# Kernel optimization log

Hardware: AMD Instinct MI355X
Metric: run time of the kernel (lower is better)

The kernel has to match this reference:

```python
import jax, jax.numpy as jnp
import numpy as np

# Module hyperparameters
P_, K_, NH = 8, 4, 8
B, H, W, C = 2, 64, 24, 256


def setup_inputs() -> dict:
    key = jax.random.key(0)
    ks = jax.random.split(key, 16)

    def w(k, shape, s=0.02):
        return (jax.random.normal(k, shape) * s).astype(jnp.float32)

    z = lambda *shape: jnp.zeros(shape, jnp.float32)
    return {
        'x_2d': jax.random.normal(ks[0], (B, H, W, C), dtype=jnp.float32),
        # block projections (used as x @ W + b)
        'wq_proj': w(ks[1], (C, C)), 'bq_proj': z(C),
        'wk_proj': w(ks[2], (C, C)), 'bk_proj': z(C),
        'wv_proj': w(ks[3], (C, C)), 'bv_proj': z(C),
        # routing attention projections
        'wq_a': w(ks[4], (C, C)), 'bq_a': z(C),
        'wk_a': w(ks[5], (C, C)), 'bk_a': z(C),
        'wv_a': w(ks[6], (C, C)), 'bv_a': z(C),
        'wo_a': w(ks[7], (C, C)), 'bo_a': z(C),
        # global conv path (HWIO, 5x5, SAME padding == torch padding=2)
        'conv_w': w(ks[8], (5, 5, C, C)), 'conv_b': z(C),
        # layer norms
        'ln1_g': jnp.ones((C,), jnp.float32), 'ln1_b': z(C),
        'ln2_g': jnp.ones((C,), jnp.float32), 'ln2_b': z(C),
    }


def _layer_norm(t, g, b, eps=1e-5):
    m = t.mean(-1, keepdims=True)
    v = ((t - m) ** 2).mean(-1, keepdims=True)
    return (t - m) / jnp.sqrt(v + eps) * g + b


def reference(x_2d, wq_proj, bq_proj, wk_proj, bk_proj, wv_proj, bv_proj,
              wq_a, bq_a, wk_a, bk_a, wv_a, bv_a, wo_a, bo_a,
              conv_w, conv_b, ln1_g, ln1_b, ln2_g, ln2_b):
    Bb, Hh, Ww, Cc = x_2d.shape
    hp = Hh // P_                      # block height
    dk = Cc // NH
    kv = min(K_, P_)

    x_p = x_2d.reshape(Bb, P_, hp, Ww, Cc)
    q_p = x_p @ wq_proj + bq_proj
    k_p = x_p @ wk_proj + bk_proj
    v_p = x_p @ wv_proj + bv_proj

    # block-level routing: mean-pooled block descriptors -> top-k blocks
    q_loc = q_p.mean((2, 3))           # [B,P,C]
    k_loc = k_p.mean((2, 3))
    S_loc = jnp.einsum('bpc,bqc->bpq', q_loc, k_loc)
    _, R = jax.lax.top_k(S_loc, kv)    # [B,P,kv] int32 indices into P

    # gather routed K/V blocks: [B,P,kv,hp*W,C]
    k_flat = k_p.reshape(Bb, P_, hp * Ww, Cc)
    v_flat = v_p.reshape(Bb, P_, hp * Ww, Cc)
    k_fil = jax.vmap(lambda t, r: t[r])(k_flat, R).reshape(Bb, P_, kv, hp, Ww, Cc)
    v_fil = jax.vmap(lambda t, r: t[r])(v_flat, R).reshape(Bb, P_, kv, hp, Ww, Cc)
    q_un = jnp.broadcast_to(q_p[:, :, None], (Bb, P_, kv, hp, Ww, Cc))

    # multi-head attention over flattened (kv*hp*W) per block p
    L = kv * hp * Ww
    def to_heads(t, w, b):
        t = t @ w + b
        t = t.reshape(Bb, P_, kv, hp, Ww, NH, dk)
        return t.transpose(0, 5, 1, 2, 3, 4, 6).reshape(Bb, NH, P_, L, dk)

    qh = to_heads(q_un, wq_a, bq_a)
    kh = to_heads(k_fil, wk_a, bk_a)
    vh = to_heads(v_fil, wv_a, bv_a)

    scores = jnp.einsum('bhpqd,bhpkd->bhpqk', qh, kh) / jnp.sqrt(jnp.float32(dk))
    attn = jax.nn.softmax(scores, axis=-1)
    ctx = jnp.einsum('bhpqk,bhpkd->bhpqd', attn, vh)
    # 'b h p (k hp w) dk -> b p k hp w (h dk)'
    ctx = ctx.reshape(Bb, NH, P_, kv, hp, Ww, dk).transpose(0, 2, 3, 4, 5, 1, 6)
    ctx = ctx.reshape(Bb, P_, kv, hp, Ww, Cc)
    routing_out = (ctx @ wo_a + bo_a).mean(2)          # [B,P,hp,W,C]

    x_res = _layer_norm(x_p + routing_out, ln1_g, ln1_b)

    # global conv path (NHWC SAME conv, kernel 5)
    kv_g = (k_p + v_p).reshape(Bb, Hh, Ww, Cc)
    g = jax.lax.conv_general_dilated(kv_g, conv_w, (1, 1), 'SAME',
                                     dimension_numbers=('NHWC', 'HWIO', 'NHWC')) + conv_b
    g = g.reshape(Bb, P_, hp, Ww, Cc)

    out = _layer_norm(x_res + g, ln2_g, ln2_b)
    return out.reshape(Bb, Hh, Ww, Cc)
```

## Files before the change

### kernel.cpp

```cpp
#include <hip/hip_runtime.h>
#include <hip/hip_bf16.h>


#define NPOS 3072
#define CD   256
#define NE   (NPOS*CD)

typedef short bf16x8 __attribute__((ext_vector_type(8)));
typedef float f32x4  __attribute__((ext_vector_type(4)));

__device__ inline ushort f2bf(float f) {
    __hip_bfloat16 h = __float2bfloat16(f);
    return *reinterpret_cast<ushort*>(&h);
}
__device__ inline float bf2f(ushort u) {
    unsigned v = ((unsigned)u) << 16;
    return *reinterpret_cast<float*>(&v);
}

__global__ __launch_bounds__(256) void wtrans7(
    const float* __restrict__ w0, const float* __restrict__ w1, const float* __restrict__ w2,
    const float* __restrict__ w3, const float* __restrict__ w4, const float* __restrict__ w5,
    const float* __restrict__ w6, ushort* __restrict__ wt)
{
    __shared__ float l[64*65];
    int mat = blockIdx.y;
    const float* Wm = mat==0?w0:mat==1?w1:mat==2?w2:mat==3?w3:mat==4?w4:mat==5?w5:w6;
    int r2 = blockIdx.x;
    int ci0 = (r2 >> 2)*64, co0 = (r2 & 3)*64;
    int tid = threadIdx.x, a = tid >> 6, c = tid & 63;
    #pragma unroll 4
    for (int k = 0; k < 16; ++k) {
        int cil = k*4 + a;
        l[cil*65 + c] = Wm[(size_t)(ci0 + cil)*256 + co0 + c];
    }
    __syncthreads();
    #pragma unroll 4
    for (int k = 0; k < 16; ++k) {
        int col = k*4 + a;
        wt[(size_t)mat*65536 + ((size_t)(co0 + col))*256 + ci0 + c] = f2bf(l[c*65 + col]);
    }
}

__global__ __launch_bounds__(256) void wtrans(
    const float* __restrict__ cw, ushort* __restrict__ wct)
{
    __shared__ float l[64*65];
    int blk = blockIdx.x;
    int tap = blk >> 4;
    int r2  = blk & 15;
    int ci0 = (r2 >> 2) * 64;
    int co0 = (r2 & 3) * 64;
    int tid = threadIdx.x;
    int a = tid >> 6;
    int c = tid & 63;
    #pragma unroll 4
    for (int k = 0; k < 16; ++k) {
        int cil = k*4 + a;
        l[cil*65 + c] = cw[(size_t)tap*65536 + (size_t)(ci0 + cil)*256 + co0 + c];
    }
    __syncthreads();
    #pragma unroll 4
    for (int k = 0; k < 16; ++k) {
        int col = k*4 + a;
        wct[((size_t)(tap*256 + co0 + col))*256 + ci0 + c] = f2bf(l[c*65 + col]);
    }
}

__global__ __launch_bounds__(256) void qkloc2(
    const float* __restrict__ x,
    const float* __restrict__ wq, const float* __restrict__ bq,
    const float* __restrict__ wk, const float* __restrict__ bk,
    float* __restrict__ qloc, float* __restrict__ kloc)
{
    __shared__ float xs[256];
    int bp = blockIdx.x, c = threadIdx.x;
    float s = 0.f;
    for (int i = 0; i < 192; ++i)
        s += x[((size_t)(bp*192 + i))*256 + c];
    xs[c] = s * (1.0f/192.0f);
    __syncthreads();
    const float* W  = blockIdx.y ? wk : wq;
    const float* Bv = blockIdx.y ? bk : bq;
    float* dst      = blockIdx.y ? kloc : qloc;
    float acc = Bv[c];
    #pragma unroll 8
    for (int k = 0; k < 256; ++k)
        acc += xs[k] * W[(size_t)k*256 + c];
    dst[bp*256 + c] = acc;
}

__global__ void topk_kern(const float* __restrict__ qloc, const float* __restrict__ kloc,
                          int* __restrict__ Rix)
{
    __shared__ float S[64];
    int b = blockIdx.x, t = threadIdx.x;
    int p = t >> 3, qq = t & 7;
    float s = 0.f;
    for (int c = 0; c < 256; ++c)
        s += qloc[(b*8+p)*256 + c] * kloc[(b*8+qq)*256 + c];
    S[t] = s;
    __syncthreads();
    if (t < 8) {
        float vals[8];
        #pragma unroll
        for (int j = 0; j < 8; ++j) vals[j] = S[t*8 + j];
        for (int j = 0; j < 4; ++j) {
            int best = 0; float bv = vals[0];
            #pragma unroll
            for (int i = 1; i < 8; ++i) if (vals[i] > bv) { bv = vals[i]; best = i; }
            Rix[(b*8 + t)*4 + j] = best;
            vals[best] = -1e30f;
        }
    }
}

__global__ __launch_bounds__(256) void gemm_btx3(
    const float* __restrict__ A,
    const ushort* __restrict__ T0, const ushort* __restrict__ T1, const ushort* __restrict__ T2,
    const float* __restrict__ B0, const float* __restrict__ B1, const float* __restrict__ B2,
    ushort* __restrict__ U0, ushort* __restrict__ U1, ushort* __restrict__ U2)
{
    __shared__ __align__(16) ushort As[32*264];
    int y = blockIdx.y;
    const ushort* T = y==0 ? T0 : (y==1 ? T1 : T2);
    const float* Bi = y==0 ? B0 : (y==1 ? B1 : B2);
    ushort* U = y==0 ? U0 : (y==1 ? U1 : U2);
    int tid = threadIdx.x;
    int m0 = blockIdx.x*32;
    #pragma unroll
    for (int i = 0; i < 4; ++i) {
        int c = i*256 + tid;
        int pos = c >> 5, off = (c & 31)*8;
        const float* src = A + (size_t)(m0 + pos)*256 + off;
        float4 v0 = *(const float4*)src;
        float4 v1 = *(const float4*)(src + 4);
        ushort4 o0, o1;
        o0.x = f2bf(v0.x); o0.y = f2bf(v0.y); o0.z = f2bf(v0.z); o0.w = f2bf(v0.w);
        o1.x = f2bf(v1.x); o1.y = f2bf(v1.y); o1.z = f2bf(v1.z); o1.w = f2bf(v1.w);
        *(ushort4*)&As[pos*264 + off]     = o0;
        *(ushort4*)&As[pos*264 + off + 4] = o1;
    }
    __syncthreads();
    int w = tid >> 6, lane = tid & 63, lm = lane & 15, lq = lane >> 4;
    const ushort* tb = T + ((size_t)(w*64 + lm))*256 + lq*8;

    f32x4 acc[2][4];
    #pragma unroll
    for (int mt = 0; mt < 2; ++mt)
        #pragma unroll
        for (int nt = 0; nt < 4; ++nt) acc[mt][nt] = (f32x4){0.f,0.f,0.f,0.f};

    bf16x8 bw[4];
    #pragma unroll
    for (int nt = 0; nt < 4; ++nt) bw[nt] = *(const bf16x8*)(tb + nt*4096);

    for (int kc = 0; kc < 8; ++kc) {
        int nk = (kc + 1 < 8) ? kc + 1 : 7;
        bf16x8 bn[4];
        #pragma unroll
        for (int nt = 0; nt < 4; ++nt) bn[nt] = *(const bf16x8*)(tb + nt*4096 + nk*32);
        bf16x8 af[2];
        #pragma unroll
        for (int mt = 0; mt < 2; ++mt)
            af[mt] = *(const bf16x8*)&As[(mt*16 + lm)*264 + kc*32 + lq*8];
        #pragma unroll
        for (int mt = 0; mt < 2; ++mt)
            #pragma unroll
            for (int nt = 0; nt < 4; ++nt)
                acc[mt][nt] = __builtin_amdgcn_mfma_f32_16x16x32_bf16(af[mt], bw[nt], acc[mt][nt], 0,0,0);
        #pragma unroll
        for (int nt = 0; nt < 4; ++nt) bw[nt] = bn[nt];
    }

    #pragma unroll
    for (int mt = 0; mt < 2; ++mt) {
        #pragma unroll
        for (int nt = 0; nt < 4; ++nt) {
            int n = w*64 + nt*16 + lm;
            float bb = Bi[n];
            #pragma unroll
            for (int j = 0; j < 4; ++j) {
                int m = m0 + mt*16 + lq*4 + j;
                U[(size_t)m*256 + n] = f2bf(acc[mt][nt][j] + bb);
            }
        }
    }
}

__global__ __launch_bounds__(256) void gemm_bt3(
    const ushort* __restrict__ A0, const ushort* __restrict__ A1, const ushort* __restrict__ A2,
    const ushort* __restrict__ T0, const ushort* __restrict__ T1, const ushort* __restrict__ T2,
    const float* __restrict__ B0, const float* __restrict__ B1, const float* __restrict__ B2,
    ushort* __restrict__ U0, ushort* __restrict__ U1, ushort* __restrict__ U2,
    float s0, float s1, float s2)
{
    __shared__ __align__(16) ushort As[32*264];
    int y = blockIdx.y;
    const ushort* A = y==0 ? A0 : (y==1 ? A1 : A2);
    const ushort* T = y==0 ? T0 : (y==1 ? T1 : T2);
    const float* Bi = y==0 ? B0 : (y==1 ? B1 : B2);
    ushort* U = y==0 ? U0 : (y==1 ? U1 : U2);
    float  sc = y==0 ? s0 : (y==1 ? s1 : s2);
    int tid = threadIdx.x;
    int m0 = blockIdx.x*32;
    #pragma unroll
    for (int i = 0; i < 4; ++i) {
        int c = i*256 + tid;
        int pos = c >> 5, off = (c & 31)*8;
        *(bf16x8*)&As[pos*264 + off] = *(const bf16x8*)(A + (size_t)(m0 + pos)*256 + off);
    }
    __syncthreads();
    int w = tid >> 6, lane = tid & 63, lm = lane & 15, lq = lane >> 4;
    const ushort* tb = T + ((size_t)(w*64 + lm))*256 + lq*8;

    f32x4 acc[2][4];
    #pragma unroll
    for (int mt = 0; mt < 2; ++mt)
        #pragma unroll
        for (int nt = 0; nt < 4; ++nt) acc[mt][nt] = (f32x4){0.f,0.f,0.f,0.f};

    bf16x8 bw[4];
    #pragma unroll
    for (int nt = 0; nt < 4; ++nt) bw[nt] = *(const bf16x8*)(tb + nt*4096);

    for (int kc = 0; kc < 8; ++kc) {
        int nk = (kc + 1 < 8) ? kc + 1 : 7;
        bf16x8 bn[4];
        #pragma unroll
        for (int nt = 0; nt < 4; ++nt) bn[nt] = *(const bf16x8*)(tb + nt*4096 + nk*32);
        bf16x8 af[2];
        #pragma unroll
        for (int mt = 0; mt < 2; ++mt)
            af[mt] = *(const bf16x8*)&As[(mt*16 + lm)*264 + kc*32 + lq*8];
        #pragma unroll
        for (int mt = 0; mt < 2; ++mt)
            #pragma unroll
            for (int nt = 0; nt < 4; ++nt)
                acc[mt][nt] = __builtin_amdgcn_mfma_f32_16x16x32_bf16(af[mt], bw[nt], acc[mt][nt], 0,0,0);
        #pragma unroll
        for (int nt = 0; nt < 4; ++nt) bw[nt] = bn[nt];
    }

    #pragma unroll
    for (int mt = 0; mt < 2; ++mt) {
        #pragma unroll
        for (int nt = 0; nt < 4; ++nt) {
            int n = w*64 + nt*16 + lm;
            float bb = Bi[n];
            #pragma unroll
            for (int j = 0; j < 4; ++j) {
                int m = m0 + mt*16 + lq*4 + j;
                U[(size_t)m*256 + n] = f2bf((acc[mt][nt][j] + bb) * sc);
            }
        }
    }
}

__global__ __launch_bounds__(256) void attn_mfma2(
    const ushort* __restrict__ qab, const ushort* __restrict__ kab,
    const ushort* __restrict__ vab, const int* __restrict__ Rix,
    float* __restrict__ pl, float* __restrict__ pacc)
{
    __shared__ ushort P[4][16*40];
    __shared__ ushort Vs[32*200];
    int tid = threadIdx.x, w = tid >> 6, lane = tid & 63;
    int lm = lane & 15, lq = lane >> 4;
    int bph = blockIdx.x, kvb = blockIdx.y;
    int bp = bph >> 3, h = bph & 7, b = bp >> 3;
    int r = Rix[bp*4 + kvb];
    int vrow0 = (b*8 + r)*192;

    #pragma unroll
    for (int i = 0; i < 6; ++i) {
        int idx = i*256 + tid;
        int pos = idx >> 3, c4 = (idx & 7)*4;
        ushort4 v = *(const ushort4*)(vab + ((size_t)(vrow0 + pos))*256 + h*32 + c4);
        Vs[(c4+0)*200 + pos] = v.x;
        Vs[(c4+1)*200 + pos] = v.y;
        Vs[(c4+2)*200 + pos] = v.z;
        Vs[(c4+3)*200 + pos] = v.w;
    }

    bf16x8 qf[3];
    #pragma unroll
    for (int t = 0; t < 3; ++t)
        qf[t] = *(const bf16x8*)(qab + ((size_t)(bp*192 + w*48 + t*16 + lm))*256 + h*32 + lq*8);

    const ushort* kbase = kab + ((size_t)(vrow0))*256 + h*32 + lq*8;
    ushort* pw = P[w];
    __syncthreads();

    f32x4 O[3][2];
    #pragma unroll
    for (int t = 0; t < 3; ++t) { O[t][0] = (f32x4){0,0,0,0}; O[t][1] = (f32x4){0,0,0,0}; }
    float l[3] = {0.f, 0.f, 0.f};

    for (int k0 = 0; k0 < 192; k0 += 32) {
        bf16x8 kf0 = *(const bf16x8*)(kbase + (size_t)(k0 + lm)*256);
        bf16x8 kf1 = *(const bf16x8*)(kbase + (size_t)(k0 + 16 + lm)*256);
        bf16x8 vf0 = *(const bf16x8*)(&Vs[lm*200 + k0 + lq*8]);
        bf16x8 vf1 = *(const bf16x8*)(&Vs[(16 + lm)*200 + k0 + lq*8]);
        #pragma unroll
        for (int t = 0; t < 3; ++t) {
            f32x4 s0 = __builtin_amdgcn_mfma_f32_16x16x32_bf16(kf0, qf[t], (f32x4){0,0,0,0}, 0,0,0);
            f32x4 s1 = __builtin_amdgcn_mfma_f32_16x16x32_bf16(kf1, qf[t], (f32x4){0,0,0,0}, 0,0,0);
            float p0[4], p1[4];
            #pragma unroll
            for (int j = 0; j < 4; ++j) { p0[j] = __expf(s0[j]); p1[j] = __expf(s1[j]); }
            l[t] += p0[0]+p0[1]+p0[2]+p0[3] + p1[0]+p1[1]+p1[2]+p1[3];
            ushort4 a, c;
            a.x = f2bf(p0[0]); a.y = f2bf(p0[1]); a.z = f2bf(p0[2]); a.w = f2bf(p0[3]);
            c.x = f2bf(p1[0]); c.y = f2bf(p1[1]); c.z = f2bf(p1[2]); c.w = f2bf(p1[3]);
            *(ushort4*)(pw + lm*40 + lq*4)      = a;
            *(ushort4*)(pw + lm*40 + 16 + lq*4) = c;
            bf16x8 pf = *(const bf16x8*)(pw + lm*40 + lq*8);
            O[t][0] = __builtin_amdgcn_mfma_f32_16x16x32_bf16(pf, vf0, O[t][0], 0,0,0);
            O[t][1] = __builtin_amdgcn_mfma_f32_16x16x32_bf16(pf, vf1, O[t][1], 0,0,0);
        }
    }

    #pragma unroll
    for (int t = 0; t < 3; ++t) {
        float lt = l[t];
        lt += __shfl_xor(lt, 16);
        lt += __shfl_xor(lt, 32);
        size_t pbase = ((size_t)(bph*4 + kvb))*192 + w*48 + t*16;
        if (lq == 0) pl[pbase + lm] = lt;
        #pragma unroll
        for (int nt = 0; nt < 2; ++nt)
            #pragma unroll
            for (int reg = 0; reg < 4; ++reg)
                pacc[(pbase + lq*4 + reg)*32 + nt*16 + lm] = O[t][nt][reg];
    }
}

__global__ __launch_bounds__(256) void gemm_wo_ln(
    const float* __restrict__ pl, const float* __restrict__ pacc,
    const ushort* __restrict__ T, const float* __restrict__ boa,
    const float* __restrict__ x,
    const float* __restrict__ g1, const float* __restrict__ b1,
    float* __restrict__ x_res)
{
    __shared__ __align__(16) ushort As[32*264];
    __shared__ float L2x[32*256];
    int tid = threadIdx.x;
    int m0 = blockIdx.x*32;
    #pragma unroll
    for (int i = 0; i < 4; ++i) {
        int c = i*256 + tid;
        int pos = c >> 5, off = (c & 31)*8;
        int m = m0 + pos;
        int bp = m / 192, q = m - bp*192;
        int h = off >> 5, d0 = off & 31;
        int bph = bp*8 + h;
        float ls = 0.f;
        float cv[8] = {0,0,0,0,0,0,0,0};
        #pragma unroll
        for (int k = 0; k < 4; ++k) {
            size_t pidx = ((size_t)(bph*4 + k))*192 + q;
            ls += pl[pidx];
            float4 a0 = *(const float4*)(pacc + pidx*32 + d0);
            float4 a1 = *(const float4*)(pacc + pidx*32 + d0 + 4);
            cv[0] += a0.x; cv[1] += a0.y; cv[2] += a0.z; cv[3] += a0.w;
            cv[4] += a1.x; cv[5] += a1.y; cv[6] += a1.z; cv[7] += a1.w;
        }
        ushort o[8];
        #pragma unroll
        for (int j = 0; j < 8; ++j) o[j] = f2bf(cv[j] / ls);
        *(ushort4*)&As[pos*264 + off]     = make_ushort4(o[0],o[1],o[2],o[3]);
        *(ushort4*)&As[pos*264 + off + 4] = make_ushort4(o[4],o[5],o[6],o[7]);
    }
    __syncthreads();
    int w = tid >> 6, lane = tid & 63, lm = lane & 15, lq = lane >> 4;
    const ushort* tb = T + ((size_t)(w*64 + lm))*256 + lq*8;

    f32x4 acc[2][4];
    #pragma unroll
    for (int mt = 0; mt < 2; ++mt)
        #pragma unroll
        for (int nt = 0; nt < 4; ++nt) acc[mt][nt] = (f32x4){0.f,0.f,0.f,0.f};

    bf16x8 bw[4];
    #pragma unroll
    for (int nt = 0; nt < 4; ++nt) bw[nt] = *(const bf16x8*)(tb + nt*4096);

    for (int kc = 0; kc < 8; ++kc) {
        int nk = (kc + 1 < 8) ? kc + 1 : 7;
        bf16x8 bn[4];
        #pragma unroll
        for (int nt = 0; nt < 4; ++nt) bn[nt] = *(const bf16x8*)(tb + nt*4096 + nk*32);
        bf16x8 af[2];
        #pragma unroll
        for (int mt = 0; mt < 2; ++mt)
            af[mt] = *(const bf16x8*)&As[(mt*16 + lm)*264 + kc*32 + lq*8];
        #pragma unroll
        for (int mt = 0; mt < 2; ++mt)
            #pragma unroll
            for (int nt = 0; nt < 4; ++nt)
                acc[mt][nt] = __builtin_amdgcn_mfma_f32_16x16x32_bf16(af[mt], bw[nt], acc[mt][nt], 0,0,0);
        #pragma unroll
        for (int nt = 0; nt < 4; ++nt) bw[nt] = bn[nt];
    }

    #pragma unroll
    for (int mt = 0; mt < 2; ++mt) {
        #pragma unroll
        for (int nt = 0; nt < 4; ++nt) {
            int n = w*64 + nt*16 + lm;
            float bb = boa[n];
            #pragma unroll
            for (int j = 0; j < 4; ++j) {
                int pos = mt*16 + lq*4 + j;
                float val = acc[mt][nt][j] + bb;
                L2x[pos*256 + n] = val + x[(size_t)(m0 + pos)*256 + n];
            }
        }
    }
    __syncthreads();
    #pragma unroll
    for (int rr = 0; rr < 8; ++rr) {
        int pos = w*8 + rr;
        float4 a = *(const float4*)(&L2x[pos*256 + lane*4]);
        float x0 = a.x, x1 = a.y, x2 = a.z, x3 = a.w;
        float s  = x0 + x1 + x2 + x3;
        float sq = x0*x0 + x1*x1 + x2*x2 + x3*x3;
        #pragma unroll
        for (int off = 32; off > 0; off >>= 1) {
            s  += __shfl_xor(s,  off);
            sq += __shfl_xor(sq, off);
        }
        float mean = s * (1.0f/256.0f);
        float var  = sq * (1.0f/256.0f) - mean*mean;
        float rstd = rsqrtf(var + 1e-5f);
        float4 gv = *(const float4*)(g1 + lane*4);
        float4 bv = *(const float4*)(b1 + lane*4);
        float4 o;
        o.x = (x0 - mean)*rstd*gv.x + bv.x;
        o.y = (x1 - mean)*rstd*gv.y + bv.y;
        o.z = (x2 - mean)*rstd*gv.z + bv.z;
        o.w = (x3 - mean)*rstd*gv.w + bv.w;
        *(float4*)(x_res + (size_t)(m0 + pos)*256 + lane*4) = o;
    }
}

__global__ __launch_bounds__(256) void addkv_pad2(
    const ushort* __restrict__ kpb, const ushort* __restrict__ vpb, ushort* __restrict__ kvb)
{
    int t  = blockIdx.x*256 + threadIdx.x;
    int ci = (t & 63) * 4;
    int p  = t >> 6;
    int xp = p % 28;
    int rr = p / 28;
    int yp = rr % 68;
    int b  = rr / 68;
    int y = yp - 2, x = xp - 2;
    ushort4 o; o.x = 0; o.y = 0; o.z = 0; o.w = 0;
    if (y >= 0 && y < 64 && x >= 0 && x < 24) {
        size_t base = ((size_t)((b*64 + y)*24 + x))*256 + ci;
        ushort4 a = *(const ushort4*)(kpb + base);
        ushort4 c = *(const ushort4*)(vpb + base);
        o.x = f2bf(bf2f(a.x) + bf2f(c.x));
        o.y = f2bf(bf2f(a.y) + bf2f(c.y));
        o.z = f2bf(bf2f(a.z) + bf2f(c.z));
        o.w = f2bf(bf2f(a.w) + bf2f(c.w));
    }
    *(ushort4*)(kvb + (size_t)p*256 + ci) = o;
}

__global__ __launch_bounds__(256) void conv_mfma5(
    const ushort* __restrict__ kvb, const ushort* __restrict__ wct,
    float* __restrict__ pconv)
{
    __shared__ __align__(16) ushort Arows[2][9504];
    int tid = threadIdx.x;
    int bid = blockIdx.x;
    int ch = bid & 1;
    int t2 = bid >> 1;
    int rp = t2 / 5, dy = t2 - rp*5;
    int b = rp >> 5, y0 = (rp & 31)*2;

    const ushort* src0 = kvb + ((size_t)((b*68 + y0 + dy)*28))*256;
    const ushort* src1 = kvb + ((size_t)((b*68 + y0 + 1 + dy)*28))*256;
    #pragma unroll
    for (int i = 0; i < 7; ++i) {
        int c = i*256 + tid;
        int row = (c >= 896);
        int cc = c - row*896;
        int pos = cc >> 5, off = (cc & 31)*8;
        *(bf16x8*)(&Arows[row][pos*264 + off]) =
            *(const bf16x8*)((row ? src1 : src0) + (size_t)(pos*256 + off));
    }
    __syncthreads();

    int w = tid >> 6;
    int lane = tid & 63, lm = lane & 15, lq = lane >> 4;
    const ushort* bbase = wct + ((size_t)((dy*5)*256 + ch*128 + w*32 + lm))*256 + lq*8;
    const ushort* a00 = &Arows[0][lm*264 + lq*8];

    f32x4 acc[2][2][2];
    #pragma unroll
    for (int r = 0; r < 2; ++r)
        #pragma unroll
        for (int mt = 0; mt < 2; ++mt)
            #pragma unroll
            for (int nt = 0; nt < 2; ++nt)
                acc[r][mt][nt] = (f32x4){0.f,0.f,0.f,0.f};

    bf16x8 b0[2], b1[2];
    #pragma unroll
    for (int nt = 0; nt < 2; ++nt) b0[nt] = *(const bf16x8*)(bbase + nt*4096);
    #pragma unroll
    for (int nt = 0; nt < 2; ++nt) b1[nt] = *(const bf16x8*)(bbase + 32 + nt*4096);

    for (int iter = 0; iter < 40; ++iter) {
        int i2 = (iter + 2 < 40) ? iter + 2 : 39;
        int boff = (i2 >> 3)*65536 + (i2 & 7)*32;
        bf16x8 bn[2];
        #pragma unroll
        for (int nt = 0; nt < 2; ++nt) bn[nt] = *(const bf16x8*)(bbase + boff + nt*4096);

        int aoff = (iter >> 3)*264 + (iter & 7)*32;
        bf16x8 af[2][2];
        #pragma unroll
        for (int r = 0; r < 2; ++r)
            #pragma unroll
            for (int mt = 0; mt < 2; ++mt)
                af[r][mt] = *(const bf16x8*)(a00 + r*9504 + mt*4224 + aoff);

        #pragma unroll
        for (int r = 0; r < 2; ++r)
            #pragma unroll
            for (int mt = 0; mt < 2; ++mt)
                #pragma unroll
                for (int nt = 0; nt < 2; ++nt)
                    acc[r][mt][nt] = __builtin_amdgcn_mfma_f32_16x16x32_bf16(
                        af[r][mt], b0[nt], acc[r][mt][nt], 0, 0, 0);

        #pragma unroll
        for (int nt = 0; nt < 2; ++nt) { b0[nt] = b1[nt]; b1[nt] = bn[nt]; }
    }

    #pragma unroll
    for (int r = 0; r < 2; ++r) {
        int grow = rp*2 + r;
        #pragma unroll
        for (int mt = 0; mt < 2; ++mt) {
            #pragma unroll
            for (int nt = 0; nt < 2; ++nt) {
                int cob = ch*128 + w*32 + nt*16 + lm;
                #pragma unroll
                for (int j = 0; j < 4; ++j) {
                    int x = mt*16 + lq*4 + j;
                    if (x < 24)
                        pconv[((size_t)(dy*3072 + grow*24 + x))*256 + cob]
                            = acc[r][mt][nt][j];
                }
            }
        }
    }
}

__global__ __launch_bounds__(256) void ln2_fused(
    const float* __restrict__ xr, const float* __restrict__ pc, const float* __restrict__ cb,
    const float* __restrict__ gamma, const float* __restrict__ beta,
    float* __restrict__ out)
{
    int pos  = blockIdx.x*4 + (threadIdx.x >> 6);
    int lane = threadIdx.x & 63;
    size_t base = (size_t)pos*256 + lane*4;
    float4 gsum = *(const float4*)(cb + lane*4);
    #pragma unroll
    for (int d = 0; d < 5; ++d) {
        float4 v = *(const float4*)(pc + (size_t)d*NE + base);
        gsum.x += v.x; gsum.y += v.y; gsum.z += v.z; gsum.w += v.w;
    }
    float4 a = *(const float4*)(xr + base);
    float x0 = a.x + gsum.x, x1 = a.y + gsum.y, x2 = a.z + gsum.z, x3 = a.w + gsum.w;
    float s  = x0 + x1 + x2 + x3;
    float sq = x0*x0 + x1*x1 + x2*x2 + x3*x3;
    #pragma unroll
    for (int off = 32; off > 0; off >>= 1) {
        s  += __shfl_xor(s,  off);
        sq += __shfl_xor(sq, off);
    }
    float mean = s * (1.0f/256.0f);
    float var  = sq * (1.0f/256.0f) - mean*mean;
    float rstd = rsqrtf(var + 1e-5f);
    float4 gv = *(const float4*)(gamma + lane*4);
    float4 bv = *(const float4*)(beta  + lane*4);
    float4 o;
    o.x = (x0 - mean)*rstd*gv.x + bv.x;
    o.y = (x1 - mean)*rstd*gv.y + bv.y;
    o.z = (x2 - mean)*rstd*gv.z + bv.z;
    o.w = (x3 - mean)*rstd*gv.w + bv.w;
    *(float4*)(out + base) = o;
}

extern "C" void kernel_launch(void* const* d_in, const int* in_sizes, int n_in,
                              void* d_out, int out_size, void* d_ws, size_t ws_size,
                              hipStream_t stream)
{
    (void)in_sizes; (void)n_in; (void)out_size; (void)ws_size;
    const float* x    = (const float*)d_in[0];
    const float* wq   = (const float*)d_in[1];
    const float* bq   = (const float*)d_in[2];
    const float* wk   = (const float*)d_in[3];
    const float* bk   = (const float*)d_in[4];
    const float* wv   = (const float*)d_in[5];
    const float* bv   = (const float*)d_in[6];
    const float* wqa  = (const float*)d_in[7];
    const float* bqa  = (const float*)d_in[8];
    const float* wka  = (const float*)d_in[9];
    const float* bka  = (const float*)d_in[10];
    const float* wva  = (const float*)d_in[11];
    const float* bva  = (const float*)d_in[12];
    const float* woa  = (const float*)d_in[13];
    const float* boa  = (const float*)d_in[14];
    const float* cw   = (const float*)d_in[15];
    const float* cbi  = (const float*)d_in[16];
    const float* ln1g = (const float*)d_in[17];
    const float* ln1b = (const float*)d_in[18];
    const float* ln2g = (const float*)d_in[19];
    const float* ln2b = (const float*)d_in[20];
    float* out = (float*)d_out;

    float* ws = (float*)d_ws;
    const size_t HNE = NE/2;
    ushort* qpb = (ushort*)(ws + 0*HNE);
    ushort* kpb = (ushort*)(ws + 1*HNE);
    ushort* xb  = (ushort*)(ws + 2*HNE);
    ushort* vpb = (ushort*)(ws + 3*HNE);
    ushort* qab = (ushort*)(ws + 4*HNE);
    ushort* kab = (ushort*)(ws + 5*HNE);
    ushort* vab = (ushort*)(ws + 6*HNE);
    float* R    = ws + 8*HNE;
    float* pacc = R;
    float* pl   = R + 3145728;
    float* pconv= R;
    ushort* wt7 = (ushort*)(R + 3932160);
    ushort* wct = (ushort*)(R + 3932160 + 229376);
    ushort* kvb = (ushort*)(R + 3932160 + 229376 + 819200);
    float* qloc = R + 3932160 + 229376 + 819200 + 487424;
    float* kloc = qloc + 4096;
    int*   Rix  = (int*)(kloc + 4096);
    float* x_res = (float*)xb;

    wtrans7<<<dim3(16,7), 256, 0, stream>>>(wq,wk,wv,wqa,wka,wva,woa, wt7);
    wtrans<<<400, 256, 0, stream>>>(cw, wct);
    qkloc2<<<dim3(16,2), 256, 0, stream>>>(x, wq,bq, wk,bk, qloc, kloc);
    topk_kern<<<2, 64, 0, stream>>>(qloc, kloc, Rix);
    gemm_btx3<<<dim3(96,3), 256, 0, stream>>>(
        x, wt7, wt7+65536, wt7+131072, bq,bk,bv, qpb,kpb,vpb);
    addkv_pad2<<<952, 256, 0, stream>>>(kpb, vpb, kvb);
    gemm_bt3<<<dim3(96,3), 256, 0, stream>>>(
        qpb,kpb,vpb, wt7+196608, wt7+262144, wt7+327680, bqa,bka,bva,
        qab,kab,vab, 0.17677669529663687f,1.f,1.f);
    attn_mfma2<<<dim3(128,4), 256, 0, stream>>>(qab, kab, vab, Rix, pl, pacc);
    gemm_wo_ln<<<96, 256, 0, stream>>>(pl, pacc, wt7+393216, boa, x, ln1g, ln1b, x_res);
    conv_mfma5<<<640, 256, 0, stream>>>(kvb, wct, pconv);
    ln2_fused<<<NPOS/4, 256, 0, stream>>>(x_res, pconv, cbi, ln2g, ln2b, out);
}
```

Measured before the change: 212.1 us.

## Fuse k+v add/pad into conv, merge weight transposes, store partials in bf16

Merges the two weight-transpose kernels into one launch. Drops the separate addkv_pad kernel by having the conv kernel load k and v directly, add them and handle the zero padding on the fly. The attention partial accumulators and the per-tap conv partials are now stored as bf16 instead of fp32, which halves that intermediate traffic. This removes two launches and a padded buffer round trip, at the cost of extra rounding in the partial sums and redundant k+v adds across conv taps.

```diff
diff --git a/kernel.cpp b/kernel.cpp
--- a/kernel.cpp
+++ b/kernel.cpp
@@ -17,53 +17,47 @@
     unsigned v = ((unsigned)u) << 16;
     return *reinterpret_cast<float*>(&v);
 }
-
-__global__ __launch_bounds__(256) void wtrans7(
+__device__ inline bf16x8 addbf(bf16x8 a, bf16x8 b) {
+    bf16x8 o;
+    #pragma unroll
+    for (int j = 0; j < 8; ++j)
+        o[j] = (short)f2bf(bf2f((ushort)a[j]) + bf2f((ushort)b[j]));
+    return o;
+}
+
+__global__ __launch_bounds__(256) void wtransA(
     const float* __restrict__ w0, const float* __restrict__ w1, const float* __restrict__ w2,
     const float* __restrict__ w3, const float* __restrict__ w4, const float* __restrict__ w5,
-    const float* __restrict__ w6, ushort* __restrict__ wt)
+    const float* __restrict__ w6, const float* __restrict__ cw,
+    ushort* __restrict__ wt, ushort* __restrict__ wct)
 {
     __shared__ float l[64*65];
-    int mat = blockIdx.y;
-    const float* Wm = mat==0?w0:mat==1?w1:mat==2?w2:mat==3?w3:mat==4?w4:mat==5?w5:w6;
-    int r2 = blockIdx.x;
+    int blk = blockIdx.x;
+    const float* M;
+    ushort* D;
+    int r2;
+    if (blk < 112) {
+        int mat = blk >> 4; r2 = blk & 15;
+        M = mat==0?w0:mat==1?w1:mat==2?w2:mat==3?w3:mat==4?w4:mat==5?w5:w6;
+        D = wt + (size_t)mat*65536;
+    } else {
+        int b2 = blk - 112;
+        int tap = b2 >> 4; r2 = b2 & 15;
+        M = cw + (size_t)tap*65536;
+        D = wct + (size_t)tap*65536;
+    }
     int ci0 = (r2 >> 2)*64, co0 = (r2 & 3)*64;
     int tid = threadIdx.x, a = tid >> 6, c = tid & 63;
     #pragma unroll 4
     for (int k = 0; k < 16; ++k) {
         int cil = k*4 + a;
-        l[cil*65 + c] = Wm[(size_t)(ci0 + cil)*256 + co0 + c];
+        l[cil*65 + c] = M[(size_t)(ci0 + cil)*256 + co0 + c];
     }
     __syncthreads();
     #pragma unroll 4
     for (int k = 0; k < 16; ++k) {
         int col = k*4 + a;
-        wt[(size_t)mat*65536 + ((size_t)(co0 + col))*256 + ci0 + c] = f2bf(l[c*65 + col]);
-    }
-}
-
-__global__ __launch_bounds__(256) void wtrans(
-    const float* __restrict__ cw, ushort* __restrict__ wct)
-{
-    __shared__ float l[64*65];
-    int blk = blockIdx.x;
-    int tap = blk >> 4;
-    int r2  = blk & 15;
-    int ci0 = (r2 >> 2) * 64;
-    int co0 = (r2 & 3) * 64;
-    int tid = threadIdx.x;
-    int a = tid >> 6;
-    int c = tid & 63;
-    #pragma unroll 4
-    for (int k = 0; k < 16; ++k) {
-        int cil = k*4 + a;
-        l[cil*65 + c] = cw[(size_t)tap*65536 + (size_t)(ci0 + cil)*256 + co0 + c];
-    }
-    __syncthreads();
-    #pragma unroll 4
-    for (int k = 0; k < 16; ++k) {
-        int col = k*4 + a;
-        wct[((size_t)(tap*256 + co0 + col))*256 + ci0 + c] = f2bf(l[c*65 + col]);
+        D[((size_t)(co0 + col))*256 + ci0 + c] = f2bf(l[c*65 + col]);
     }
 }
 
@@ -260,7 +254,7 @@
 __global__ __launch_bounds__(256) void attn_mfma2(
     const ushort* __restrict__ qab, const ushort* __restrict__ kab,
     const ushort* __restrict__ vab, const int* __restrict__ Rix,
-    float* __restrict__ pl, float* __restrict__ pacc)
+    float* __restrict__ pl, ushort* __restrict__ pacc)
 {
     __shared__ ushort P[4][16*40];
     __shared__ ushort Vs[32*200];
@@ -331,12 +325,12 @@
         for (int nt = 0; nt < 2; ++nt)
             #pragma unroll
             for (int reg = 0; reg < 4; ++reg)
-                pacc[(pbase + lq*4 + reg)*32 + nt*16 + lm] = O[t][nt][reg];
+                pacc[(pbase + lq*4 + reg)*32 + nt*16 + lm] = f2bf(O[t][nt][reg]);
     }
 }
 
 __global__ __launch_bounds__(256) void gemm_wo_ln(
-    const float* __restrict__ pl, const float* __restrict__ pacc,
+    const float* __restrict__ pl, const ushort* __restrict__ pacc,
     const ushort* __restrict__ T, const float* __restrict__ boa,
     const float* __restrict__ x,
     const float* __restrict__ g1, const float* __restrict__ b1,
@@ -360,10 +354,9 @@
         for (int k = 0; k < 4; ++k) {
             size_t pidx = ((size_t)(bph*4 + k))*192 + q;
             ls += pl[pidx];
-            float4 a0 = *(const float4*)(pacc + pidx*32 + d0);
-            float4 a1 = *(const float4*)(pacc + pidx*32 + d0 + 4);
-            cv[0] += a0.x; cv[1] += a0.y; cv[2] += a0.z; cv[3] += a0.w;
-            cv[4] += a1.x; cv[5] += a1.y; cv[6] += a1.z; cv[7] += a1.w;
+            bf16x8 pv = *(const bf16x8*)(pacc + pidx*32 + d0);
+            #pragma unroll
+            for (int j = 0; j < 8; ++j) cv[j] += bf2f((ushort)pv[j]);
         }
         ushort o[8];
         #pragma unroll
@@ -444,33 +437,9 @@
     }
 }
 
-__global__ __launch_bounds__(256) void addkv_pad2(
-    const ushort* __restrict__ kpb, const ushort* __restrict__ vpb, ushort* __restrict__ kvb)
-{
-    int t  = blockIdx.x*256 + threadIdx.x;
-    int ci = (t & 63) * 4;
-    int p  = t >> 6;
-    int xp = p % 28;
-    int rr = p / 28;
-    int yp = rr % 68;
-    int b  = rr / 68;
-    int y = yp - 2, x = xp - 2;
-    ushort4 o; o.x = 0; o.y = 0; o.z = 0; o.w = 0;
-    if (y >= 0 && y < 64 && x >= 0 && x < 24) {
-        size_t base = ((size_t)((b*64 + y)*24 + x))*256 + ci;
-        ushort4 a = *(const ushort4*)(kpb + base);
-        ushort4 c = *(const ushort4*)(vpb + base);
-        o.x = f2bf(bf2f(a.x) + bf2f(c.x));
-        o.y = f2bf(bf2f(a.y) + bf2f(c.y));
-        o.z = f2bf(bf2f(a.z) + bf2f(c.z));
-        o.w = f2bf(bf2f(a.w) + bf2f(c.w));
-    }
-    *(ushort4*)(kvb + (size_t)p*256 + ci) = o;
-}
-
-__global__ __launch_bounds__(256) void conv_mfma5(
-    const ushort* __restrict__ kvb, const ushort* __restrict__ wct,
-    float* __restrict__ pconv)
+__global__ __launch_bounds__(256) void conv_mfma6(
+    const ushort* __restrict__ kpb, const ushort* __restrict__ vpb,
+    const ushort* __restrict__ wct, ushort* __restrict__ pconv)
 {
     __shared__ __align__(16) ushort Arows[2][9504];
     int tid = threadIdx.x;
@@ -480,16 +449,20 @@
     int rp = t2 / 5, dy = t2 - rp*5;
     int b = rp >> 5, y0 = (rp & 31)*2;
 
-    const ushort* src0 = kvb + ((size_t)((b*68 + y0 + dy)*28))*256;
-    const ushort* src1 = kvb + ((size_t)((b*68 + y0 + 1 + dy)*28))*256;
+    const bf16x8 zero8 = (bf16x8){0,0,0,0,0,0,0,0};
     #pragma unroll
     for (int i = 0; i < 7; ++i) {
         int c = i*256 + tid;
         int row = (c >= 896);
         int cc = c - row*896;
         int pos = cc >> 5, off = (cc & 31)*8;
-        *(bf16x8*)(&Arows[row][pos*264 + off]) =
-            *(const bf16x8*)((row ? src1 : src0) + (size_t)(pos*256 + off));
+        int y = y0 + row + dy - 2;
+        bf16x8 v = zero8;
+        if (y >= 0 && y < 64 && pos >= 2 && pos < 26) {
+            size_t sb = ((size_t)((b*64 + y)*24 + (pos - 2)))*256 + off;
+            v = addbf(*(const bf16x8*)(kpb + sb), *(const bf16x8*)(vpb + sb));
+        }
+        *(bf16x8*)(&Arows[row][pos*264 + off]) = v;
     }
     __syncthreads();
 
@@ -554,7 +527,7 @@
                     int x = mt*16 + lq*4 + j;
                     if (x < 24)
                         pconv[((size_t)(dy*3072 + grow*24 + x))*256 + cob]
-                            = acc[r][mt][nt][j];
+                            = f2bf(acc[r][mt][nt][j]);
                 }
             }
         }
@@ -562,7 +535,7 @@
 }
 
 __global__ __launch_bounds__(256) void ln2_fused(
-    const float* __restrict__ xr, const float* __restrict__ pc, const float* __restrict__ cb,
+    const float* __restrict__ xr, const ushort* __restrict__ pc, const float* __restrict__ cb,
     const float* __restrict__ gamma, const float* __restrict__ beta,
     float* __restrict__ out)
 {
@@ -572,8 +545,9 @@
     float4 gsum = *(const float4*)(cb + lane*4);
     #pragma unroll
     for (int d = 0; d < 5; ++d) {
-        float4 v = *(const float4*)(pc + (size_t)d*NE + base);
-        gsum.x += v.x; gsum.y += v.y; gsum.z += v.z; gsum.w += v.w;
+        ushort4 v = *(const ushort4*)(pc + (size_t)d*NE + base);
+        gsum.x += bf2f(v.x); gsum.y += bf2f(v.y);
+        gsum.z += bf2f(v.z); gsum.w += bf2f(v.w);
     }
     float4 a = *(const float4*)(xr + base);
     float x0 = a.x + gsum.x, x1 = a.y + gsum.y, x2 = a.z + gsum.z, x3 = a.w + gsum.w;
@@ -629,35 +603,31 @@
     const size_t HNE = NE/2;
     ushort* qpb = (ushort*)(ws + 0*HNE);
     ushort* kpb = (ushort*)(ws + 1*HNE);
-    ushort* xb  = (ushort*)(ws + 2*HNE);
     ushort* vpb = (ushort*)(ws + 3*HNE);
     ushort* qab = (ushort*)(ws + 4*HNE);
     ushort* kab = (ushort*)(ws + 5*HNE);
     ushort* vab = (ushort*)(ws + 6*HNE);
+    float* x_res = (float*)(ws + 6*HNE);
     float* R    = ws + 8*HNE;
-    float* pacc = R;
-    float* pl   = R + 3145728;
-    float* pconv= R;
+    ushort* pacc = (ushort*)R;
+    float*  pl   = R + 1572864;
+    ushort* pconv= (ushort*)R;
     ushort* wt7 = (ushort*)(R + 3932160);
     ushort* wct = (ushort*)(R + 3932160 + 229376);
-    ushort* kvb = (ushort*)(R + 3932160 + 229376 + 819200);
-    float* qloc = R + 3932160 + 229376 + 819200 + 487424;
+    float* qloc = R + 3932160 + 229376 + 819200;
     float* kloc = qloc + 4096;
     int*   Rix  = (int*)(kloc + 4096);
-    float* x_res = (float*)xb;
-
-    wtrans7<<<dim3(16,7), 256, 0, stream>>>(wq,wk,wv,wqa,wka,wva,woa, wt7);
-    wtrans<<<400, 256, 0, stream>>>(cw, wct);
+
+    wtransA<<<512, 256, 0, stream>>>(wq,wk,wv,wqa,wka,wva,woa, cw, wt7, wct);
     qkloc2<<<dim3(16,2), 256, 0, stream>>>(x, wq,bq, wk,bk, qloc, kloc);
     topk_kern<<<2, 64, 0, stream>>>(qloc, kloc, Rix);
     gemm_btx3<<<dim3(96,3), 256, 0, stream>>>(
         x, wt7, wt7+65536, wt7+131072, bq,bk,bv, qpb,kpb,vpb);
-    addkv_pad2<<<952, 256, 0, stream>>>(kpb, vpb, kvb);
     gemm_bt3<<<dim3(96,3), 256, 0, stream>>>(
         qpb,kpb,vpb, wt7+196608, wt7+262144, wt7+327680, bqa,bka,bva,
         qab,kab,vab, 0.17677669529663687f,1.f,1.f);
     attn_mfma2<<<dim3(128,4), 256, 0, stream>>>(qab, kab, vab, Rix, pl, pacc);
     gemm_wo_ln<<<96, 256, 0, stream>>>(pl, pacc, wt7+393216, boa, x, ln1g, ln1b, x_res);
-    conv_mfma5<<<640, 256, 0, stream>>>(kvb, wct, pconv);
+    conv_mfma6<<<640, 256, 0, stream>>>(kpb, vpb, wct, pconv);
     ln2_fused<<<NPOS/4, 256, 0, stream>>>(x_res, pconv, cbi, ln2g, ln2b, out);
 }
```

Result: faster. 205.9 us (-2.9%).
